# Kernel tuning notes

Hardware: AMD Instinct MI355X
Metric: run time of the kernel (lower is better)

The kernel has to match this reference:

```python
import jax, jax.numpy as jnp
import numpy as np

N_CLUSTERS = 16
CLUSTER_SIZE = 32
N_HIDDEN = 16
N_FEATURES = N_CLUSTERS * CLUSTER_SIZE  # 512
BATCH = 131072


def setup_inputs() -> dict:
    key = jax.random.key(0)
    k_x, k_perm, k_ew, k_eb, k_dw, k_db = jax.random.split(key, 6)
    x = jax.random.normal(k_x, (BATCH, N_FEATURES), dtype=jnp.float32)
    # disjoint random feature clusters (a permutation split into groups)
    clusters = jax.random.permutation(k_perm, N_FEATURES).reshape(
        N_CLUSTERS, CLUSTER_SIZE).astype(jnp.int32)
    s_e = 1.0 / np.sqrt(CLUSTER_SIZE)
    s_d = 1.0 / np.sqrt(N_HIDDEN)
    enc_w = jax.random.uniform(k_ew, (N_CLUSTERS, N_HIDDEN, CLUSTER_SIZE),
                               minval=-s_e, maxval=s_e, dtype=jnp.float32)
    enc_b = jax.random.uniform(k_eb, (N_CLUSTERS, N_HIDDEN),
                               minval=-s_e, maxval=s_e, dtype=jnp.float32)
    dec_w = jax.random.uniform(k_dw, (N_CLUSTERS, CLUSTER_SIZE, N_HIDDEN),
                               minval=-s_d, maxval=s_d, dtype=jnp.float32)
    dec_b = jax.random.uniform(k_db, (N_CLUSTERS, CLUSTER_SIZE),
                               minval=-s_d, maxval=s_d, dtype=jnp.float32)
    return {"x": x, "clusters": clusters, "enc_w": enc_w, "enc_b": enc_b,
            "dec_w": dec_w, "dec_b": dec_b}


def reference(x, clusters, enc_w, enc_b, dec_w, dec_b):
    # gather per-cluster feature columns: [B, nC, cs]
    xi = x[:, clusters]
    # encoder: Linear(cs -> h) per cluster
    h = jnp.einsum('bnc,nhc->bnh', xi, enc_w) + enc_b  # [B, nC, h]
    # decoder: Linear(h -> cs) per cluster
    y = jnp.einsum('bnh,nch->bnc', h, dec_w) + dec_b   # [B, nC, cs]
    # concat cluster outputs along feature dim (cluster order)
    return y.reshape(x.shape[0], -1)  # [B, nC*cs]
```

## Files before the change

kernel.cpp:

```cpp
#include <hip/hip_runtime.h>


#define B_ROWS   131072
#define F        512
#define NC       16
#define CS       32
#define NH       16
#define NBLOCKS  1024
#define RPB      128
#define RPI      8
#define NITER    (RPB / RPI)

__global__ __launch_bounds__(256, 4)
void ensemble_kernel(const float* __restrict__ x,
                     const int*   __restrict__ clusters,
                     const float* __restrict__ enc_w,
                     const float* __restrict__ enc_b,
                     const float* __restrict__ dec_w,
                     const float* __restrict__ dec_b,
                     float*       __restrict__ out) {
    __shared__ float s_xi[RPI][F];
    __shared__ int   s_tgt[F];

    const int t = threadIdx.x;

    for (int j = t; j < F; j += 256) {
        int col = clusters[j];
        int nn = j >> 5, cc = j & 31;
        s_tgt[col] = (nn << 5) | ((cc + (nn << 2)) & 31);
    }
    __syncthreads();

    const int cbase = (t & 127) << 2;
    const int tgt0 = s_tgt[cbase + 0];
    const int tgt1 = s_tgt[cbase + 1];
    const int tgt2 = s_tgt[cbase + 2];
    const int tgt3 = s_tgt[cbase + 3];

    const int n  = t >> 4;
    const int c0 = (t & 15) << 1;

    float m0[32], m1[32];
    #pragma unroll
    for (int i = 0; i < 32; ++i) { m0[i] = 0.f; m1[i] = 0.f; }
    float b0 = dec_b[n * CS + c0];
    float b1 = dec_b[n * CS + c0 + 1];

    for (int h = 0; h < NH; ++h) {
        const float d0 = dec_w[(n * CS + c0)     * NH + h];
        const float d1 = dec_w[(n * CS + c0 + 1) * NH + h];
        const float eb = enc_b[n * NH + h];
        b0 += d0 * eb;
        b1 += d1 * eb;
        const float4* ew = (const float4*)(enc_w + (n * NH + h) * CS);
        #pragma unroll
        for (int k = 0; k < 8; ++k) {
            float4 e = ew[k];
            m0[4*k+0] += d0 * e.x;  m1[4*k+0] += d1 * e.x;
            m0[4*k+1] += d0 * e.y;  m1[4*k+1] += d1 * e.y;
            m0[4*k+2] += d0 * e.z;  m1[4*k+2] += d1 * e.z;
            m0[4*k+3] += d0 * e.w;  m1[4*k+3] += d1 * e.w;
        }
    }

    const int rhalf = t >> 7;
    const int row_block = blockIdx.x * RPB;
    const int xioff = n << 5;

    for (int it = 0; it < NITER; ++it) {
        const int r0 = row_block + it * RPI;

        float4 v[4];
        #pragma unroll
        for (int p = 0; p < 4; ++p) {
            const float* src = x + (size_t)(r0 + p * 2 + rhalf) * F + cbase;
            v[p] = *(const float4*)src;
        }

        __syncthreads();

        #pragma unroll
        for (int p = 0; p < 4; ++p) {
            float* dst = s_xi[p * 2 + rhalf];
            dst[tgt0] = v[p].x;
            dst[tgt1] = v[p].y;
            dst[tgt2] = v[p].z;
            dst[tgt3] = v[p].w;
        }

        __syncthreads();

        #pragma unroll
        for (int r = 0; r < RPI; ++r) {
            float a0 = b0, a1 = b1;
            const float* xr = &s_xi[r][xioff];
            #pragma unroll
            for (int k = 0; k < 8; ++k) {
                const int kk = (k + n) & 7;
                float4 xv = *(const float4*)(xr + (kk << 2));
                a0 += m0[4*k+0] * xv.x;  a1 += m1[4*k+0] * xv.x;
                a0 += m0[4*k+1] * xv.y;  a1 += m1[4*k+1] * xv.y;
                a0 += m0[4*k+2] * xv.z;  a1 += m1[4*k+2] * xv.z;
                a0 += m0[4*k+3] * xv.w;  a1 += m1[4*k+3] * xv.w;
            }
            float2 o = make_float2(a0, a1);
            *(float2*)(out + (size_t)(r0 + r) * F + xioff + c0) = o;
        }
    }
}

extern "C" void kernel_launch(void* const* d_in, const int* in_sizes, int n_in,
                              void* d_out, int out_size, void* d_ws, size_t ws_size,
                              hipStream_t stream) {
    const float* x      = (const float*)d_in[0];
    const int*   clus   = (const int*)  d_in[1];
    const float* enc_w  = (const float*)d_in[2];
    const float* enc_b  = (const float*)d_in[3];
    const float* dec_w  = (const float*)d_in[4];
    const float* dec_b  = (const float*)d_in[5];
    float*       out    = (float*)d_out;

    ensemble_kernel<<<NBLOCKS, 256, 0, stream>>>(x, clus, enc_w, enc_b, dec_w, dec_b, out);
}
```

Before: 478.0 us.

## Double-buffer shared x tile and prefetch next rows during compute

Splits the shared staging buffer into two halves of four rows each. The next tile's global loads are issued before computing on the current tile, and the first tile's loads are hoisted above the weight-fusion prologue. This cuts the number of barriers per tile from two to one and hides global load latency behind the FMA work. In exchange it uses smaller tiles, so there are twice as many iterations, and the compute body is duplicated for the epilogue.

```diff
diff --git a/kernel.cpp b/kernel.cpp
--- a/kernel.cpp
+++ b/kernel.cpp
@@ -8,7 +8,7 @@
 #define NH       16
 #define NBLOCKS  1024
 #define RPB      128
-#define RPI      8
+#define RPI      4
 #define NITER    (RPB / RPI)
 
 __global__ __launch_bounds__(256, 4)
@@ -19,7 +19,7 @@
                      const float* __restrict__ dec_w,
                      const float* __restrict__ dec_b,
                      float*       __restrict__ out) {
-    __shared__ float s_xi[RPI][F];
+    __shared__ float s_xi[2][RPI][F];
     __shared__ int   s_tgt[F];
 
     const int t = threadIdx.x;
@@ -39,6 +39,17 @@
 
     const int n  = t >> 4;
     const int c0 = (t & 15) << 1;
+    const int rhalf = t >> 7;
+    const int row_block = blockIdx.x * RPB;
+
+    const float* xp = x + (size_t)(row_block + rhalf) * F + cbase;
+    const int xioff = n << 5;
+    float* op = out + (size_t)row_block * F + xioff + c0;
+
+    float4 v[2];
+    v[0] = *(const float4*)(xp);
+    v[1] = *(const float4*)(xp + 2 * F);
+    xp += RPI * F;
 
     float m0[32], m1[32];
     #pragma unroll
@@ -63,37 +74,25 @@
         }
     }
 
-    const int rhalf = t >> 7;
-    const int row_block = blockIdx.x * RPB;
-    const int xioff = n << 5;
+    {
+        float* d0p = s_xi[0][0 * 2 + rhalf];
+        d0p[tgt0] = v[0].x; d0p[tgt1] = v[0].y; d0p[tgt2] = v[0].z; d0p[tgt3] = v[0].w;
+        float* d1p = s_xi[0][1 * 2 + rhalf];
+        d1p[tgt0] = v[1].x; d1p[tgt1] = v[1].y; d1p[tgt2] = v[1].z; d1p[tgt3] = v[1].w;
+    }
+    __syncthreads();
 
-    for (int it = 0; it < NITER; ++it) {
-        const int r0 = row_block + it * RPI;
+    for (int it = 0; it < NITER - 1; ++it) {
+        const int cur = it & 1;
 
-        float4 v[4];
-        #pragma unroll
-        for (int p = 0; p < 4; ++p) {
-            const float* src = x + (size_t)(r0 + p * 2 + rhalf) * F + cbase;
-            v[p] = *(const float4*)src;
-        }
-
-        __syncthreads();
-
-        #pragma unroll
-        for (int p = 0; p < 4; ++p) {
-            float* dst = s_xi[p * 2 + rhalf];
-            dst[tgt0] = v[p].x;
-            dst[tgt1] = v[p].y;
-            dst[tgt2] = v[p].z;
-            dst[tgt3] = v[p].w;
-        }
-
-        __syncthreads();
+        v[0] = *(const float4*)(xp);
+        v[1] = *(const float4*)(xp + 2 * F);
+        xp += RPI * F;
 
         #pragma unroll
         for (int r = 0; r < RPI; ++r) {
             float a0 = b0, a1 = b1;
-            const float* xr = &s_xi[r][xioff];
+            const float* xr = &s_xi[cur][r][xioff];
             #pragma unroll
             for (int k = 0; k < 8; ++k) {
                 const int kk = (k + n) & 7;
@@ -103,8 +102,35 @@
                 a0 += m0[4*k+2] * xv.z;  a1 += m1[4*k+2] * xv.z;
                 a0 += m0[4*k+3] * xv.w;  a1 += m1[4*k+3] * xv.w;
             }
-            float2 o = make_float2(a0, a1);
-            *(float2*)(out + (size_t)(r0 + r) * F + xioff + c0) = o;
+            *(float2*)(op + r * F) = make_float2(a0, a1);
+        }
+        op += RPI * F;
+
+        {
+            float* d0p = s_xi[cur ^ 1][0 * 2 + rhalf];
+            d0p[tgt0] = v[0].x; d0p[tgt1] = v[0].y; d0p[tgt2] = v[0].z; d0p[tgt3] = v[0].w;
+            float* d1p = s_xi[cur ^ 1][1 * 2 + rhalf];
+            d1p[tgt0] = v[1].x; d1p[tgt1] = v[1].y; d1p[tgt2] = v[1].z; d1p[tgt3] = v[1].w;
+        }
+        __syncthreads();
+    }
+
+    {
+        const int cur = (NITER - 1) & 1;
+        #pragma unroll
+        for (int r = 0; r < RPI; ++r) {
+            float a0 = b0, a1 = b1;
+            const float* xr = &s_xi[cur][r][xioff];
+            #pragma unroll
+            for (int k = 0; k < 8; ++k) {
+                const int kk = (k + n) & 7;
+                float4 xv = *(const float4*)(xr + (kk << 2));
+                a0 += m0[4*k+0] * xv.x;  a1 += m1[4*k+0] * xv.x;
+                a0 += m0[4*k+1] * xv.y;  a1 += m1[4*k+1] * xv.y;
+                a0 += m0[4*k+2] * xv.z;  a1 += m1[4*k+2] * xv.z;
+                a0 += m0[4*k+3] * xv.w;  a1 += m1[4*k+3] * xv.w;
+            }
+            *(float2*)(op + r * F) = make_float2(a0, a1);
         }
     }
 }
```

New measurement: 470.8 us. Within noise of the previous version (-1.5%).
